# Kernel optimization log

Measured on AMD Instinct MI355X. Metric: run time of the kernel, lower is better.

The kernel has to match this reference:

```python
import jax, jax.numpy as jnp
import numpy as np

N = 4096     # nagents
OBS = 256    # obs_size
HID = 256    # hid_size
G = 64       # gat_hid_size
H1 = 4       # gat_num_heads (so H1*G == HID)
H2 = 1       # gat_num_heads_out
A = 64       # actions
QMAX = 255.0  # 2**quant_bits - 1, quant_min = 0
NEG_SLOPE = 0.2


def _lstm_cell(x, h, c, Wih, Whh, bih, bhh):
    gates = x @ Wih.T + bih + h @ Whh.T + bhh
    i, f, g, o = jnp.split(gates, 4, axis=-1)
    c2 = jax.nn.sigmoid(f) * c + jax.nn.sigmoid(i) * jnp.tanh(g)
    h2 = jax.nn.sigmoid(o) * jnp.tanh(c2)
    return h2, c2


def _gat(x, adj, W, a_i, a_j, b, average, self_loop_type):
    # x: [n, in], adj: [n, n], W: [in, H*g], a_i/a_j: [H, g], b: [H*g] or [g_out]
    n = x.shape[0]
    H, g = a_i.shape
    eye = jnp.eye(n, dtype=adj.dtype)
    if self_loop_type == 1:      # force self-loops
        adj = adj * (1.0 - eye) + eye
    elif self_loop_type == 2:    # remove self-loops
        adj = adj * (1.0 - eye)
    h = (x @ W).reshape(n, H, g)                      # [n, H, g]
    ci = jnp.einsum('nhg,hg->hn', h, a_i)             # [H, n]
    cj = jnp.einsum('nhg,hg->hn', h, a_j)             # [H, n]
    e = jax.nn.leaky_relu(ci[:, :, None] + cj[:, None, :], NEG_SLOPE)  # [H, n, n]
    att = jax.nn.softmax(jnp.where(adj[None] > 0, e, -9e15), axis=-1) * adj[None]
    out = jnp.einsum('hij,jhg->ihg', att, h)          # [n, H, g]
    out = out.mean(axis=1) if average else out.reshape(n, H * g)
    return out + b


def _fake_quant(t, bmask):
    # dynamic-range fake quantization over masked entries (min/max detached)
    big = jnp.asarray(1e30, t.dtype)
    mn = jax.lax.stop_gradient(jnp.min(jnp.where(bmask, t, big)))
    mx = jax.lax.stop_gradient(jnp.max(jnp.where(bmask, t, -big)))
    eq = mn == mx
    mn = jnp.where(eq, mn - 0.01, mn)
    mx = jnp.where(eq, mx + 0.01, mx)
    scale = (mx - mn) / QMAX
    zp = jnp.round(-mn / scale)  # quant_min = 0
    deq = (jnp.clip(jnp.round(t / scale + zp), 0.0, QMAX) - zp) * scale
    return jnp.where(bmask, deq, t)


def _qloss(t, bmask):
    return jnp.sum(jnp.where(bmask, jnp.log2(2.0 * QMAX * jnp.abs(t) + 1.0), 0.0))


def _forward(obs, h0, c0, Wobs, bobs, Wih, Whh, bih, bhh,
             W1, ai1, aj1, b1, W2, ai2, aj2, b2, Wv, bv, Wa, ba):
    n = N
    mask = jnp.ones((n, 1), obs.dtype)        # all agents alive
    enc = obs.reshape(n, -1) @ Wobs + bobs    # obs encoder, squeeze batch=1
    h, c = _lstm_cell(enc, h0, c0, Wih, Whh, bih, bhh)
    comm = h
    bmask = jnp.broadcast_to(mask > 0, comm.shape)
    comm = _fake_quant(comm, bmask)
    loss = _qloss(comm, bmask)
    comm = comm * mask
    adj = jnp.ones((n, n), obs.dtype) * mask * mask.T   # complete graph
    comm = _gat(comm, adj, W1, ai1, aj1, b1, average=False, self_loop_type=1)
    comm = jax.nn.elu(comm)
    bmask2 = jnp.broadcast_to(mask > 0, comm.shape)
    comm = _fake_quant(comm, bmask2)
    loss = loss + _qloss(comm, bmask2)
    comm = _gat(comm, adj, W2, ai2, aj2, b2, average=True, self_loop_type=1)
    comm = comm * mask
    value = jnp.concatenate([h, comm], axis=-1) @ Wv + bv              # [n, 1]
    feat = jnp.concatenate([h.reshape(1, n, -1), comm.reshape(1, n, -1)], axis=-1)
    logp = jax.nn.log_softmax(feat @ Wa + ba, axis=-1)                 # [1, n, A]
    return logp, value, h, c, loss


def setup_inputs() -> dict:
    key = jax.random.key(0)
    ks = jax.random.split(key, 21)
    def rn(k, shape, sc=0.05):
        return jax.random.normal(k, shape, dtype=jnp.float32) * sc
    return {
        'obs': rn(ks[0], (1, N, OBS), 1.0),
        'h0': rn(ks[1], (N, HID), 1.0),
        'c0': rn(ks[2], (N, HID), 1.0),
        'Wobs': rn(ks[3], (OBS, HID)),
        'bobs': rn(ks[4], (HID,)),
        'Wih': rn(ks[5], (4 * HID, HID)),
        'Whh': rn(ks[6], (4 * HID, HID)),
        'bih': rn(ks[7], (4 * HID,)),
        'bhh': rn(ks[8], (4 * HID,)),
        'W1': rn(ks[9], (HID, H1 * G)),
        'ai1': rn(ks[10], (H1, G)),
        'aj1': rn(ks[11], (H1, G)),
        'b1': rn(ks[12], (H1 * G,)),
        'W2': rn(ks[13], (H1 * G, H2 * HID)),
        'ai2': rn(ks[14], (H2, HID)),
        'aj2': rn(ks[15], (H2, HID)),
        'b2': rn(ks[16], (HID,)),
        'Wv': rn(ks[17], (2 * HID, 1)),
        'bv': rn(ks[18], (1,)),
        'Wa': rn(ks[19], (2 * HID, A)),
        'ba': rn(ks[20], (A,)),
    }


def reference(obs, h0, c0, Wobs, bobs, Wih, Whh, bih, bhh,
              W1, ai1, aj1, b1, W2, ai2, aj2, b2, Wv, bv, Wa, ba):
    return _forward(obs, h0, c0, Wobs, bobs, Wih, Whh, bih, bhh,
                    W1, ai1, aj1, b1, W2, ai2, aj2, b2, Wv, bv, Wa, ba)
```

## Files before the change

kernel.cpp:

```cpp
#include <hip/hip_runtime.h>
#include <math.h>

typedef __attribute__((ext_vector_type(8))) short short8;
typedef __attribute__((ext_vector_type(4))) float floatx4;

__device__ __forceinline__ ushort f2b(float f) {
  unsigned u = __float_as_uint(f);
  unsigned r = u + 0x7FFFu + ((u >> 16) & 1u);
  return (ushort)(r >> 16);
}

__global__ __launch_bounds__(256) void prep_kernel(
    const float* __restrict__ obs, ushort* __restrict__ obs_bf,
    const float* __restrict__ h0, ushort* __restrict__ h0_bf,
    const float* __restrict__ Wih, ushort* __restrict__ Wih_bf,
    const float* __restrict__ Whh, ushort* __restrict__ Whh_bf,
    const float* __restrict__ Wobs, ushort* __restrict__ WobsT,
    const float* __restrict__ W1, ushort* __restrict__ W1T,
    const float* __restrict__ W2, ushort* __restrict__ W2T,
    const float* __restrict__ Wa, const float* __restrict__ Wv,
    const float* __restrict__ ba, const float* __restrict__ bv,
    const float* __restrict__ bih, const float* __restrict__ bhh,
    ushort* __restrict__ WaTe, float* __restrict__ bias_ext, float* __restrict__ bias12)
{
  __shared__ float tile[32][33];
  const int bid = blockIdx.x;
  const int tid = threadIdx.x;
  if (bid < 1024) {
    const int q0 = 262144, q1 = 262144, q2 = 65536, q3 = 65536;
    const int tot = q0 + q1 + q2 + q3;
    for (int idx = bid * 256 + tid; idx < tot; idx += 1024 * 256) {
      const float* s; ushort* d; size_t soff, doff; int i = idx;
      if (i < q0) { s = obs; d = obs_bf; soff = doff = (size_t)i * 4; }
      else if ((i -= q0) < q1) { s = h0; d = h0_bf; soff = doff = (size_t)i * 4; }
      else if ((i -= q1) < q2) {
        const int pr = i >> 6, k4 = i & 63;
        const int orow = (pr & 3) * 256 + (pr >> 2);
        s = Wih; d = Wih_bf; soff = (size_t)orow * 256 + k4 * 4; doff = (size_t)pr * 256 + k4 * 4;
      } else {
        i -= q2;
        const int pr = i >> 6, k4 = i & 63;
        const int orow = (pr & 3) * 256 + (pr >> 2);
        s = Whh; d = Whh_bf; soff = (size_t)orow * 256 + k4 * 4; doff = (size_t)pr * 256 + k4 * 4;
      }
      const float4 v = *(const float4*)(s + soff);
      ushort4 o; o.x = f2b(v.x); o.y = f2b(v.y); o.z = f2b(v.z); o.w = f2b(v.w);
      *(ushort4*)(d + doff) = o;
    }
  } else if (bid < 1216) {
    const int t = bid - 1024;
    const int mat = t >> 6, sub = t & 63;
    const float* in = mat == 0 ? Wobs : (mat == 1 ? W1 : W2);
    ushort* outp = mat == 0 ? WobsT : (mat == 1 ? W1T : W2T);
    const int c0 = (sub & 7) * 32, r0 = (sub >> 3) * 32;
    const int tx = tid & 31, ty = tid >> 5;
    #pragma unroll
    for (int p = 0; p < 32; p += 8)
      tile[ty + p][tx] = in[(size_t)(r0 + ty + p) * 256 + c0 + tx];
    __syncthreads();
    #pragma unroll
    for (int p = 0; p < 32; p += 8)
      outp[(size_t)(c0 + ty + p) * 256 + r0 + tx] = f2b(tile[tx][ty + p]);
  } else {
    const int idx = (bid - 1216) * 256 + tid;
    if (idx < 65536) {
      const int n = idx >> 9, k = idx & 511;
      const float v = n < 64 ? Wa[(size_t)k * 64 + n] : (n == 64 ? Wv[k] : 0.0f);
      WaTe[idx] = f2b(v);
    } else if (idx < 65536 + 128) {
      const int n = idx - 65536;
      bias_ext[n] = n < 64 ? ba[n] : (n == 64 ? bv[0] : 0.0f);
    } else if (idx < 65536 + 128 + 1024) {
      const int pc = idx - 65536 - 128;
      const int orow = (pc & 3) * 256 + (pc >> 2);
      bias12[pc] = bih[orow] + bhh[orow];
    }
  }
}

template<int BM, int BN, bool OUT_BF16>
__global__ __launch_bounds__(256) void mfma_gemm(
    const ushort* __restrict__ A1, int lda1,
    const ushort* __restrict__ B1, int ldb1, int K1,
    const ushort* __restrict__ A2, int lda2,
    const ushort* __restrict__ B2, int ldb2, int K2,
    const float* __restrict__ bias,
    void* __restrict__ Cv, int N)
{
  constexpr int LDT = 40;
  __shared__ __align__(16) ushort As[BM * LDT];
  __shared__ __align__(16) ushort Bs[BN * LDT];
  const int tid = threadIdx.x;
  const int wave = tid >> 6, lane = tid & 63;
  const int wr = wave >> 1, wc = wave & 1;
  const int m0 = blockIdx.y * BM, n0 = blockIdx.x * BN;
  constexpr int MI = BM / 32;
  constexpr int NI = BN / 32;
  floatx4 acc[MI][NI] = {};
  const int r = tid >> 2, kq = tid & 3;
  const int lm = lane & 15, lq = lane >> 4;
  const int Ktot = K1 + K2;
  for (int k0 = 0; k0 < Ktot; k0 += 32) {
    const ushort* A; const ushort* B; int lda, ldb, kk;
    if (k0 < K1) { A = A1; B = B1; lda = lda1; ldb = ldb1; kk = k0; }
    else         { A = A2; B = B2; lda = lda2; ldb = ldb2; kk = k0 - K1; }
    #pragma unroll
    for (int p = 0; p < BM / 64; ++p) {
      const int rr = r + p * 64;
      *(float4*)&As[rr * LDT + kq * 8] =
          *(const float4*)&A[(size_t)(m0 + rr) * lda + kk + kq * 8];
    }
    #pragma unroll
    for (int p = 0; p < BN / 64; ++p) {
      const int rr = r + p * 64;
      *(float4*)&Bs[rr * LDT + kq * 8] =
          *(const float4*)&B[(size_t)(n0 + rr) * ldb + kk + kq * 8];
    }
    __syncthreads();
    short8 af[MI], bfr[NI];
    #pragma unroll
    for (int i = 0; i < MI; ++i)
      af[i] = *(const short8*)&As[(wr * (BM / 2) + i * 16 + lm) * LDT + lq * 8];
    #pragma unroll
    for (int j = 0; j < NI; ++j)
      bfr[j] = *(const short8*)&Bs[(wc * (BN / 2) + j * 16 + lm) * LDT + lq * 8];
    #pragma unroll
    for (int i = 0; i < MI; ++i)
      #pragma unroll
      for (int j = 0; j < NI; ++j)
        acc[i][j] = __builtin_amdgcn_mfma_f32_16x16x32_bf16(af[i], bfr[j], acc[i][j], 0, 0, 0);
    __syncthreads();
  }
  #pragma unroll
  for (int i = 0; i < MI; ++i) {
    #pragma unroll
    for (int j = 0; j < NI; ++j) {
      const int col = n0 + wc * (BN / 2) + j * 16 + lm;
      const float badd = bias ? bias[col] : 0.0f;
      #pragma unroll
      for (int t = 0; t < 4; ++t) {
        const int row = m0 + wr * (BM / 2) + i * 16 + lq * 4 + t;
        const float v = acc[i][j][t] + badd;
        if (OUT_BF16) ((ushort*)Cv)[(size_t)row * N + col] = f2b(v);
        else          ((float*)Cv)[(size_t)row * N + col] = v;
      }
    }
  }
}

__global__ __launch_bounds__(256) void gates_lstm_kernel(
    const ushort* __restrict__ enc_bf, const ushort* __restrict__ Wihp,
    const ushort* __restrict__ h0_bf, const ushort* __restrict__ Whhp,
    const float* __restrict__ bias12p, const float* __restrict__ c0,
    float* __restrict__ h_out, float* __restrict__ c_out, ushort* __restrict__ h_bf,
    float* __restrict__ pmn, float* __restrict__ pmx)
{
  constexpr int LDT = 40;
  __shared__ __align__(16) ushort As[128 * LDT];
  __shared__ __align__(16) ushort Bs[128 * LDT];
  __shared__ __align__(16) float gbuf[64][132];
  __shared__ float smn[4], smx[4];
  const int tid = threadIdx.x;
  const int wave = tid >> 6, lane = tid & 63;
  const int wr = wave >> 1, wc = wave & 1;
  const int m0 = blockIdx.y * 128, n0 = blockIdx.x * 128;
  floatx4 acc[4][4] = {};
  const int r = tid >> 2, kq = tid & 3;
  const int lm = lane & 15, lq = lane >> 4;
  for (int k0 = 0; k0 < 512; k0 += 32) {
    const ushort* A; const ushort* B; int kk;
    if (k0 < 256) { A = enc_bf; B = Wihp; kk = k0; }
    else          { A = h0_bf;  B = Whhp; kk = k0 - 256; }
    #pragma unroll
    for (int p = 0; p < 2; ++p) {
      const int rr = r + p * 64;
      *(float4*)&As[rr * LDT + kq * 8] =
          *(const float4*)&A[(size_t)(m0 + rr) * 256 + kk + kq * 8];
      *(float4*)&Bs[rr * LDT + kq * 8] =
          *(const float4*)&B[(size_t)(n0 + rr) * 256 + kk + kq * 8];
    }
    __syncthreads();
    short8 af[4], bfr[4];
    #pragma unroll
    for (int i = 0; i < 4; ++i)
      af[i] = *(const short8*)&As[(wr * 64 + i * 16 + lm) * LDT + lq * 8];
    #pragma unroll
    for (int j = 0; j < 4; ++j)
      bfr[j] = *(const short8*)&Bs[(wc * 64 + j * 16 + lm) * LDT + lq * 8];
    #pragma unroll
    for (int i = 0; i < 4; ++i)
      #pragma unroll
      for (int j = 0; j < 4; ++j)
        acc[i][j] = __builtin_amdgcn_mfma_f32_16x16x32_bf16(af[i], bfr[j], acc[i][j], 0, 0, 0);
    __syncthreads();
  }
  float mnl = 3.0e38f, mxl = -3.0e38f;
  const int rr = tid >> 2;
  const int dd0 = (tid & 3) * 8;
  #pragma unroll
  for (int half = 0; half < 2; ++half) {
    if (wr == half) {
      #pragma unroll
      for (int i = 0; i < 4; ++i)
        #pragma unroll
        for (int j = 0; j < 4; ++j) {
          const int col = wc * 64 + j * 16 + lm;
          const float badd = bias12p[n0 + col];
          #pragma unroll
          for (int t = 0; t < 4; ++t)
            gbuf[i * 16 + lq * 4 + t][col] = acc[i][j][t] + badd;
        }
    }
    __syncthreads();
    const int ig = m0 + half * 64 + rr;
    #pragma unroll
    for (int eh = 0; eh < 2; ++eh) {
      const int ddb = dd0 + eh * 4;
      const size_t off = (size_t)ig * 256 + (n0 >> 2) + ddb;
      const float4 c4 = *(const float4*)&c0[off];
      float4 hv, cv; ushort4 hb;
      #pragma unroll
      for (int q = 0; q < 4; ++q) {
        const float4 g4 = *(const float4*)&gbuf[rr][(ddb + q) * 4];
        const float cc = ((const float*)&c4)[q];
        const float si = 1.0f / (1.0f + expf(-g4.x));
        const float sf = 1.0f / (1.0f + expf(-g4.y));
        const float so = 1.0f / (1.0f + expf(-g4.w));
        const float c2 = sf * cc + si * tanhf(g4.z);
        const float h2 = so * tanhf(c2);
        ((float*)&hv)[q] = h2; ((float*)&cv)[q] = c2; ((ushort*)&hb)[q] = f2b(h2);
        mnl = fminf(mnl, h2); mxl = fmaxf(mxl, h2);
      }
      *(float4*)&h_out[off] = hv;
      *(float4*)&c_out[off] = cv;
      *(ushort4*)&h_bf[off] = hb;
    }
    __syncthreads();
  }
  #pragma unroll
  for (int o = 32; o > 0; o >>= 1) {
    mnl = fminf(mnl, __shfl_xor(mnl, o));
    mxl = fmaxf(mxl, __shfl_xor(mxl, o));
  }
  if (lane == 0) { smn[wave] = mnl; smx[wave] = mxl; }
  __syncthreads();
  if (tid == 0) {
    const int bid = blockIdx.y * 8 + blockIdx.x;
    pmn[bid] = fminf(fminf(smn[0], smn[1]), fminf(smn[2], smn[3]));
    pmx[bid] = fmaxf(fmaxf(smx[0], smx[1]), fmaxf(smx[2], smx[3]));
  }
}

// ... 33 lines not shown
      d1 = (qq - zp) * scale; lsum += log2f(510.0f * fabsf(d1) + 1.0f); }
    { float qq = fminf(fmaxf(rintf(t.z / scale + zp), 0.0f), 255.0f);
      d2 = (qq - zp) * scale; lsum += log2f(510.0f * fabsf(d2) + 1.0f); }
    { float qq = fminf(fmaxf(rintf(t.w / scale + zp), 0.0f), 255.0f);
      d3 = (qq - zp) * scale; lsum += log2f(510.0f * fabsf(d3) + 1.0f); }
    ushort4 o; o.x = f2b(d0); o.y = f2b(d1); o.z = f2b(d2); o.w = f2b(d3);
    *(ushort4*)(q + (size_t)idx * 4) = o;
  }
  #pragma unroll
  for (int o = 32; o > 0; o >>= 1) lsum += __shfl_xor(lsum, o);
  if ((threadIdx.x & 63) == 0) sl[threadIdx.x >> 6] = lsum;
  __syncthreads();
  if (threadIdx.x == 0) part[blockIdx.x] = sl[0] + sl[1] + sl[2] + sl[3];
}

__global__ __launch_bounds__(256) void cicj1_kernel(
    const float* __restrict__ h1, const float* __restrict__ ai, const float* __restrict__ aj,
    float* __restrict__ ci, float* __restrict__ cj)
{
  const int w = threadIdx.x >> 6, lane = threadIdx.x & 63;
  const int i = blockIdx.x * 4 + w;
  #pragma unroll
  for (int hd = 0; hd < 4; ++hd) {
    const float v = h1[(size_t)i * 256 + hd * 64 + lane];
    float pi = v * ai[hd * 64 + lane];
    float pj = v * aj[hd * 64 + lane];
    #pragma unroll
    for (int o = 32; o > 0; o >>= 1) { pi += __shfl_xor(pi, o); pj += __shfl_xor(pj, o); }
    if (lane == 0) { ci[hd * 4096 + i] = pi; cj[hd * 4096 + i] = pj; }
  }
}

__global__ __launch_bounds__(256) void cicj2_kernel(
    const float* __restrict__ h2, const float* __restrict__ ai, const float* __restrict__ aj,
    float* __restrict__ ci, float* __restrict__ cj)
{
  const int w = threadIdx.x >> 6, lane = threadIdx.x & 63;
  const int i = blockIdx.x * 4 + w;
  float pi = 0.f, pj = 0.f;
  #pragma unroll
  for (int r = 0; r < 4; ++r) {
    const float v = h2[(size_t)i * 256 + r * 64 + lane];
    pi += v * ai[r * 64 + lane];
    pj += v * aj[r * 64 + lane];
  }
  #pragma unroll
  for (int o = 32; o > 0; o >>= 1) { pi += __shfl_xor(pi, o); pj += __shfl_xor(pj, o); }
  if (lane == 0) { ci[i] = pi; cj[i] = pj; }
}

__global__ __launch_bounds__(1024) void rank_sort_kernel(
    const float* __restrict__ c, float* __restrict__ sc, int* __restrict__ pm)
{
  __shared__ unsigned long long lk[4096];
  __shared__ int scnt[16][64];
  const int head = blockIdx.x >> 6;
  const int seg = blockIdx.x & 63;
  const float* ch = c + head * 4096;
  for (int idx = threadIdx.x; idx < 4096; idx += 1024) {
    unsigned u = __float_as_uint(ch[idx]);
    u = (u & 0x80000000u) ? ~u : (u | 0x80000000u);
    lk[idx] = ((unsigned long long)u << 12) | (unsigned)idx;
  }
  __syncthreads();
  const int jl = threadIdx.x & 63;
  const int kg = threadIdx.x >> 6;
  const unsigned long long my = lk[seg * 64 + jl];
  int cnt = 0;
  const int k0 = kg * 256;
  #pragma unroll 8
  for (int k = k0; k < k0 + 256; ++k)
    cnt += lk[k] < my ? 1 : 0;
  scnt[kg][jl] = cnt;
  __syncthreads();
  if (threadIdx.x < 64) {
    int rank = 0;
    #pragma unroll
    for (int g = 0; g < 16; ++g) rank += scnt[g][threadIdx.x];
    const unsigned long long kk = lk[seg * 64 + threadIdx.x];
    unsigned u = (unsigned)(kk >> 12);
    const float v = __uint_as_float((u & 0x80000000u) ? (u & 0x7fffffffu) : ~u);
    sc[head * 4096 + rank] = v;
    pm[head * 4096 + rank] = (int)(kk & 0xFFFu);
  }
}

__global__ __launch_bounds__(128) void local_scan1(
    const float* __restrict__ h1, const float* __restrict__ sc, const int* __restrict__ pm,
    float* __restrict__ PUl, float* __restrict__ PVl,
    float* __restrict__ dUl, float* __restrict__ dVl,
    float* __restrict__ cku, float* __restrict__ ckv,
    float* __restrict__ ckus, float* __restrict__ ckvs)
{
  const int head = blockIdx.x >> 6;
  const int chunk = blockIdx.x & 63;
  const int wave = threadIdx.x >> 6;
  const int lane = threadIdx.x & 63;
  const float cmax = sc[head * 4096 + 4095];
// ... 153 lines not shown
    const float us = ckus[lane];
    float iv = vs, iu = us;
    #pragma unroll
    for (int o = 1; o < 64; o <<= 1) {
      const float tv = __shfl_up(iv, o), tu = __shfl_up(iu, o);
      if (lane >= o) { iv += tv; iu += tu; }
    }
    prefVs[lane] = iv - vs;
    const float totU = __shfl(iu, 63);
    sufUs[lane] = totU - iu + us;
    if (lane == 63) { prefVs[64] = iv; sufUs[64] = 0.f; }
  }
}

__global__ __launch_bounds__(256) void combine1_kernel(
    const float* __restrict__ ci, const float* __restrict__ sc,
    const float* __restrict__ sufU, const float* __restrict__ prefV,
    const float* __restrict__ sufUs, const float* __restrict__ prefVs,
    const float* __restrict__ PUl, const float* __restrict__ PVl,
    const float* __restrict__ dUl, const float* __restrict__ dVl,
    const float* __restrict__ b1, float* __restrict__ out,
    float* __restrict__ pmn, float* __restrict__ pmx)
{
  const int i = blockIdx.x;
  const int head = threadIdx.x >> 6;
  const int lane = threadIdx.x & 63;
  const float* sch = sc + head * 4096;
  const float civ = ci[head * 4096 + i];
  const float cmax = sch[4095];
  const float sarg = civ + cmax;
  const float m = sarg > 0.f ? sarg : 0.2f * sarg;
  const float Af = expf(sarg - m);
  const float Bf = expf(0.2f * sarg - m);
  const float t = -civ;
  int lo = 0, hi = 4096;
  while (lo < hi) {
    const int mid = (lo + hi) >> 1;
    if (sch[mid] > t) hi = mid; else lo = mid + 1;
  }
  const int s = lo;
  float accP, accN, dP, dN;
  if (s == 4096) {
    accP = 0.f; dP = 0.f;
    accN = prefV[(head * 65 + 64) * 64 + lane];
    dN = prefVs[head * 65 + 64];
  } else {
    const int cs = s >> 6;
    accP = sufU[(head * 65 + cs + 1) * 64 + lane] + PUl[(size_t)(head * 4096 + s) * 64 + lane];
    accN = prefV[(head * 65 + cs) * 64 + lane] + PVl[(size_t)(head * 4096 + s) * 64 + lane];
    dP = sufUs[head * 65 + cs + 1] + dUl[head * 4096 + s];
    dN = prefVs[head * 65 + cs] + dVl[head * 4096 + s];
  }
  const float num = Af * accP + Bf * accN;
// ... 5 lines not shown
  #pragma unroll
  for (int of = 32; of > 0; of >>= 1) {
    mn = fminf(mn, __shfl_xor(mn, of));
    mx = fmaxf(mx, __shfl_xor(mx, of));
  }
  __shared__ float smn[4], smx[4];
  if (lane == 0) { smn[head] = mn; smx[head] = mx; }
  __syncthreads();
  if (threadIdx.x == 0) {
    pmn[i] = fminf(fminf(smn[0], smn[1]), fminf(smn[2], smn[3]));
    pmx[i] = fmaxf(fmaxf(smx[0], smx[1]), fmaxf(smx[2], smx[3]));
  }
}

__global__ __launch_bounds__(256) void combine2_kernel(
    const float* __restrict__ ci, const float* __restrict__ sc,
    const float* __restrict__ sufU, const float* __restrict__ prefV,
    const float* __restrict__ sufUs, const float* __restrict__ prefVs,
    const float* __restrict__ PUl, const float* __restrict__ PVl,
    const float* __restrict__ dUl, const float* __restrict__ dVl,
    const float* __restrict__ b2, ushort* __restrict__ outb)
{
  const int i = blockIdx.x;
  const int col = threadIdx.x;
  const float civ = ci[i];
  const float cmax = sc[4095];
  const float sarg = civ + cmax;
  const float m = sarg > 0.f ? sarg : 0.2f * sarg;
  const float Af = expf(sarg - m);
  const float Bf = expf(0.2f * sarg - m);
  const float t = -civ;
  int lo = 0, hi = 4096;
  while (lo < hi) {
    const int mid = (lo + hi) >> 1;
    if (sc[mid] > t) hi = mid; else lo = mid + 1;
  }
  const int s = lo;
  float accP, accN, dP, dN;
  if (s == 4096) {
    accP = 0.f; dP = 0.f;
    accN = prefV[64 * 256 + col];
    dN = prefVs[64];
  } else {
    const int cs = s >> 6;
    accP = sufU[(cs + 1) * 256 + col] + PUl[(size_t)s * 256 + col];
    accN = prefV[cs * 256 + col] + PVl[(size_t)s * 256 + col];
    dP = sufUs[cs + 1] + dUl[s];
    dN = prefVs[cs] + dVl[s];
  }
  const float num = Af * accP + Bf * accN;
// ... 107 lines not shown

  float* out       = (float*)d_out;
  float* out_logp  = out;
  float* out_value = out + 262144;
  float* out_h     = out + 266240;
  float* out_c     = out + 1314816;
  float* out_loss  = out + 2363392;

  char* ws = (char*)d_ws;
  float* part1  = (float*)(ws + 256);
  float* part2  = (float*)(ws + 1280);
  float* pmn    = (float*)(ws + 2304);
  float* pmx    = (float*)(ws + 18688);
  const size_t MB = 1048576;
  const size_t base = 35072;
  ushort* obs_bf  = (ushort*)(ws + base);
  ushort* h0_bf   = (ushort*)(ws + base + 2 * MB);
  ushort* Wih_bf  = (ushort*)(ws + base + 4 * MB);
  ushort* Whh_bf  = (ushort*)(ws + base + 4 * MB + 524288);
  ushort* WobsT   = (ushort*)(ws + base + 5 * MB);
  ushort* W1T     = (ushort*)(ws + base + 5 * MB + 131072);
  ushort* W2T     = (ushort*)(ws + base + 5 * MB + 262144);
  ushort* WaTe    = (ushort*)(ws + base + 5 * MB + 393216);
  float*  bias_ext= (float*) (ws + base + 5 * MB + 524288);
  float*  bias12  = (float*) (ws + base + 5 * MB + 525312);
  ushort* enc_bf  = (ushort*)(ws + base + 6 * MB);
  ushort* h_bf    = (ushort*)(ws + base + 8 * MB);
  ushort* comm_q1 = (ushort*)(ws + base + 10 * MB);
  ushort* comm_q2 = (ushort*)(ws + base + 12 * MB);
  ushort* comm2_bf= (ushort*)(ws + base + 14 * MB);
  float*  scratch = (float*) (ws + base + 16 * MB);
  float*  h1      = scratch;
  float*  comm1e  = (float*)((char*)scratch + 4 * MB);
  float*  h2b     = (float*)((char*)scratch + 8 * MB);
  size_t so = base + 32 * MB;
  auto alloc = [&](size_t bytes) { size_t r = so; so += (bytes + 255) & ~255ull; return (char*)ws + r; };
  float* ci1    = (float*)alloc(4 * 4096 * 4);
  float* cj1    = (float*)alloc(4 * 4096 * 4);
  float* sc1    = (float*)alloc(4 * 4096 * 4);
  int*   pm1    = (int*)  alloc(4 * 4096 * 4);
  float* cku1   = (float*)alloc(4 * 64 * 64 * 4);
  float* ckv1   = (float*)alloc(4 * 64 * 64 * 4);
  float* ckus1  = (float*)alloc(4 * 64 * 4);
  float* ckvs1  = (float*)alloc(4 * 64 * 4);
  float* sufU1  = (float*)alloc(4 * 65 * 64 * 4);
  float* prefV1 = (float*)alloc(4 * 65 * 64 * 4);
  float* sufUs1 = (float*)alloc(4 * 65 * 4);
  float* prefVs1= (float*)alloc(4 * 65 * 4);
  float* ci2    = (float*)alloc(4096 * 4);
  float* cj2    = (float*)alloc(4096 * 4);
  float* sc2    = (float*)alloc(4096 * 4);
  int*   pm2    = (int*)  alloc(4096 * 4);
  float* cku2   = (float*)alloc(64 * 256 * 4);
  float* ckv2   = (float*)alloc(64 * 256 * 4);
  float* ckus2  = (float*)alloc(64 * 4);
  float* ckvs2  = (float*)alloc(64 * 4);
  float* sufU2  = (float*)alloc(65 * 256 * 4);
  float* prefV2 = (float*)alloc(65 * 256 * 4);
  float* sufUs2 = (float*)alloc(65 * 4);
  float* prefVs2= (float*)alloc(65 * 4);
  float* PUl    = (float*)alloc(4 * 4096 * 64 * 4);
  float* PVl    = (float*)alloc(4 * 4096 * 64 * 4);
  float* dUl    = (float*)alloc(4 * 4096 * 4);
  float* dVl    = (float*)alloc(4 * 4096 * 4);

  const dim3 b256(256);
  const int N4 = 262144;

  prep_kernel<<<dim3(1477), b256, 0, stream>>>(
      obs, obs_bf, h0, h0_bf, Wih, Wih_bf, Whh, Whh_bf,
      Wobs, WobsT, W1, W1T, W2, W2T,
      Wa, Wv, ba, bv, bih, bhh, WaTe, bias_ext, bias12);
  mfma_gemm<64, 64, true><<<dim3(4, 64), b256, 0, stream>>>(
      obs_bf, 256, WobsT, 256, 256, nullptr, 0, nullptr, 0, 0, bobs, enc_bf, 256);
  gates_lstm_kernel<<<dim3(8, 32), b256, 0, stream>>>(
      enc_bf, Wih_bf, h0_bf, Whh_bf, bias12, c0, out_h, out_c, h_bf, pmn, pmx);
  quant_kernel<<<dim3(256), b256, 0, stream>>>(
      (const float4*)out_h, comm_q1, N4, pmn, pmx, 256, part1);
  mfma_gemm<64, 64, false><<<dim3(4, 64), b256, 0, stream>>>(
      comm_q1, 256, W1T, 256, 256, nullptr, 0, nullptr, 0, 0, nullptr, h1, 256);
  cicj1_kernel<<<dim3(1024), b256, 0, stream>>>(h1, ai1, aj1, ci1, cj1);
  rank_sort_kernel<<<dim3(256), dim3(1024), 0, stream>>>(cj1, sc1, pm1);
  local_scan1<<<dim3(256), dim3(128), 0, stream>>>(h1, sc1, pm1,
      PUl, PVl, dUl, dVl, cku1, ckv1, ckus1, ckvs1);
  prefix1_kernel<<<dim3(4), dim3(64), 0, stream>>>(cku1, ckv1, ckus1, ckvs1,
                                                   sufU1, prefV1, sufUs1, prefVs1);
  combine1_kernel<<<dim3(4096), b256, 0, stream>>>(ci1, sc1,
      sufU1, prefV1, sufUs1, prefVs1, PUl, PVl, dUl, dVl, b1, comm1e, pmn, pmx);
  quant_kernel<<<dim3(256), b256, 0, stream>>>(
      (const float4*)comm1e, comm_q2, N4, pmn, pmx, 4096, part2);
  mfma_gemm<64, 64, false><<<dim3(4, 64), b256, 0, stream>>>(
      comm_q2, 256, W2T, 256, 256, nullptr, 0, nullptr, 0, 0, nullptr, h2b, 256);
  cicj2_kernel<<<dim3(1024), b256, 0, stream>>>(h2b, ai2, aj2, ci2, cj2);
  rank_sort_kernel<<<dim3(64), dim3(1024), 0, stream>>>(cj2, sc2, pm2);
  local_scan2<<<dim3(2, 64), b256, 0, stream>>>(h2b, sc2, pm2,
      PUl, PVl, dUl, dVl, cku2, ckv2, ckus2, ckvs2);
  prefix2_kernel<<<dim3(1), b256, 0, stream>>>(cku2, ckv2, ckus2, ckvs2,
                                               sufU2, prefV2, sufUs2, prefVs2);
  combine2_kernel<<<dim3(4096), b256, 0, stream>>>(ci2, sc2,
      sufU2, prefV2, sufUs2, prefVs2, PUl, PVl, dUl, dVl, b2, comm2_bf);
  heads_kernel<<<dim3(64), b256, 0, stream>>>(
      h_bf, comm2_bf, WaTe, bias_ext, out_logp, out_value, part1, part2, out_loss);
}
```

Before: 245.6 us.

## Fuse bf16 casts into GEMMs, fold attention vectors into weights, register LSTM epilogue

The obs and h0 bf16 conversions now happen inside the encoder and gates GEMM tile loads, so the standalone conversion passes and their buffers go away. The attention projection vectors are folded into the GAT weights (W·a) during prep. A new gat_feat kernel then computes the features and the ci/cj coefficients together, which removes the separate cicj kernels. The gate weight permutation is changed so each lane holds all four gates in registers, dropping the shared-memory gbuf epilogue. The sort now emits integer keys so the combine binary search compares unsigned keys. This risks small numeric differences, because ci/cj now come from bf16-folded weights instead of the fp32 features.

```diff
diff --git a/kernel.cpp b/kernel.cpp
--- a/kernel.cpp
+++ b/kernel.cpp
@@ -9,46 +9,44 @@
   unsigned r = u + 0x7FFFu + ((u >> 16) & 1u);
   return (ushort)(r >> 16);
 }
+__device__ __forceinline__ unsigned encf(float f) {
+  unsigned u = __float_as_uint(f);
+  return (u & 0x80000000u) ? ~u : (u | 0x80000000u);
+}
+__device__ __forceinline__ float b2f(ushort b) {
+  return __uint_as_float(((unsigned)b) << 16);
+}
 
 __global__ __launch_bounds__(256) void prep_kernel(
-    const float* __restrict__ obs, ushort* __restrict__ obs_bf,
-    const float* __restrict__ h0, ushort* __restrict__ h0_bf,
-    const float* __restrict__ Wih, ushort* __restrict__ Wih_bf,
-    const float* __restrict__ Whh, ushort* __restrict__ Whh_bf,
+    const float* __restrict__ Wih, ushort* __restrict__ Wihp,
+    const float* __restrict__ Whh, ushort* __restrict__ Whhp,
     const float* __restrict__ Wobs, ushort* __restrict__ WobsT,
     const float* __restrict__ W1, ushort* __restrict__ W1T,
     const float* __restrict__ W2, ushort* __restrict__ W2T,
     const float* __restrict__ Wa, const float* __restrict__ Wv,
     const float* __restrict__ ba, const float* __restrict__ bv,
     const float* __restrict__ bih, const float* __restrict__ bhh,
-    ushort* __restrict__ WaTe, float* __restrict__ bias_ext, float* __restrict__ bias12)
+    ushort* __restrict__ WaTe, float* __restrict__ bias_ext, float* __restrict__ bias12,
+    const float* __restrict__ ai1, const float* __restrict__ aj1,
+    const float* __restrict__ ai2, const float* __restrict__ aj2,
+    ushort* __restrict__ wab1, ushort* __restrict__ wab2)
 {
   __shared__ float tile[32][33];
   const int bid = blockIdx.x;
   const int tid = threadIdx.x;
-  if (bid < 1024) {
-    const int q0 = 262144, q1 = 262144, q2 = 65536, q3 = 65536;
-    const int tot = q0 + q1 + q2 + q3;
-    for (int idx = bid * 256 + tid; idx < tot; idx += 1024 * 256) {
-      const float* s; ushort* d; size_t soff, doff; int i = idx;
-      if (i < q0) { s = obs; d = obs_bf; soff = doff = (size_t)i * 4; }
-      else if ((i -= q0) < q1) { s = h0; d = h0_bf; soff = doff = (size_t)i * 4; }
-      else if ((i -= q1) < q2) {
-        const int pr = i >> 6, k4 = i & 63;
-        const int orow = (pr & 3) * 256 + (pr >> 2);
-        s = Wih; d = Wih_bf; soff = (size_t)orow * 256 + k4 * 4; doff = (size_t)pr * 256 + k4 * 4;
-      } else {
-        i -= q2;
-        const int pr = i >> 6, k4 = i & 63;
-        const int orow = (pr & 3) * 256 + (pr >> 2);
-        s = Whh; d = Whh_bf; soff = (size_t)orow * 256 + k4 * 4; doff = (size_t)pr * 256 + k4 * 4;
-      }
-      const float4 v = *(const float4*)(s + soff);
-      ushort4 o; o.x = f2b(v.x); o.y = f2b(v.y); o.z = f2b(v.z); o.w = f2b(v.w);
-      *(ushort4*)(d + doff) = o;
-    }
-  } else if (bid < 1216) {
-    const int t = bid - 1024;
+  if (bid < 512) {
+    const int i = bid * 256 + tid;
+    const int half = i >> 16;
+    const int ii = i & 65535;
+    const int pr = ii >> 6, k4 = ii & 63;
+    const int orow = ((pr >> 4) & 3) * 256 + (pr >> 6) * 16 + (pr & 15);
+    const float* s = half ? Whh : Wih;
+    ushort* d = half ? Whhp : Wihp;
+    const float4 v = *(const float4*)(s + (size_t)orow * 256 + k4 * 4);
+    ushort4 o; o.x = f2b(v.x); o.y = f2b(v.y); o.z = f2b(v.z); o.w = f2b(v.w);
+    *(ushort4*)(d + (size_t)pr * 256 + k4 * 4) = o;
+  } else if (bid < 704) {
+    const int t = bid - 512;
     const int mat = t >> 6, sub = t & 63;
     const float* in = mat == 0 ? Wobs : (mat == 1 ? W1 : W2);
     ushort* outp = mat == 0 ? WobsT : (mat == 1 ? W1T : W2T);
@@ -61,8 +59,8 @@
     #pragma unroll
     for (int p = 0; p < 32; p += 8)
       outp[(size_t)(c0 + ty + p) * 256 + r0 + tx] = f2b(tile[tx][ty + p]);
-  } else {
-    const int idx = (bid - 1216) * 256 + tid;
+  } else if (bid < 965) {
+    const int idx = (bid - 704) * 256 + tid;
     if (idx < 65536) {
       const int n = idx >> 9, k = idx & 511;
       const float v = n < 64 ? Wa[(size_t)k * 64 + n] : (n == 64 ? Wv[k] : 0.0f);
@@ -72,85 +70,92 @@
       bias_ext[n] = n < 64 ? ba[n] : (n == 64 ? bv[0] : 0.0f);
     } else if (idx < 65536 + 128 + 1024) {
       const int pc = idx - 65536 - 128;
-      const int orow = (pc & 3) * 256 + (pc >> 2);
+      const int orow = ((pc >> 4) & 3) * 256 + (pc >> 6) * 16 + (pc & 15);
       bias12[pc] = bih[orow] + bhh[orow];
     }
-  }
-}
-
-template<int BM, int BN, bool OUT_BF16>
-__global__ __launch_bounds__(256) void mfma_gemm(
-    const ushort* __restrict__ A1, int lda1,
-    const ushort* __restrict__ B1, int ldb1, int K1,
-    const ushort* __restrict__ A2, int lda2,
-    const ushort* __restrict__ B2, int ldb2, int K2,
-    const float* __restrict__ bias,
-    void* __restrict__ Cv, int N)
+  } else if (bid < 981) {
+    const int c = bid - 965;
+    const int k = tid;
+    float val = 0.0f;
+    if (c < 8) {
+      const int h = c & 3;
+      const float* av = (c < 4) ? ai1 : aj1;
+      for (int g = 0; g < 64; ++g)
+        val += W1[(size_t)k * 256 + h * 64 + g] * av[h * 64 + g];
+    }
+    wab1[c * 256 + k] = f2b(val);
+  } else {
+    const int c = bid - 981;
+    const int k = tid;
+    float val = 0.0f;
+    if (c < 2) {
+      const float* av = (c == 0) ? ai2 : aj2;
+      for (int g = 0; g < 256; ++g)
+        val += W2[(size_t)k * 256 + g] * av[g];
+    }
+    wab2[c * 256 + k] = f2b(val);
+  }
+}
+
+__global__ __launch_bounds__(256) void enc_gemm(
+    const float* __restrict__ obs, const ushort* __restrict__ WobsT,
+    const float* __restrict__ bobs, ushort* __restrict__ enc_bf)
 {
   constexpr int LDT = 40;
-  __shared__ __align__(16) ushort As[BM * LDT];
-  __shared__ __align__(16) ushort Bs[BN * LDT];
+  __shared__ __align__(16) ushort As[64 * LDT];
+  __shared__ __align__(16) ushort Bs[64 * LDT];
   const int tid = threadIdx.x;
   const int wave = tid >> 6, lane = tid & 63;
   const int wr = wave >> 1, wc = wave & 1;
-  const int m0 = blockIdx.y * BM, n0 = blockIdx.x * BN;
-  constexpr int MI = BM / 32;
-  constexpr int NI = BN / 32;
-  floatx4 acc[MI][NI] = {};
+  const int m0 = blockIdx.y * 64, n0 = blockIdx.x * 64;
+  floatx4 acc[2][2] = {};
   const int r = tid >> 2, kq = tid & 3;
   const int lm = lane & 15, lq = lane >> 4;
-  const int Ktot = K1 + K2;
-  for (int k0 = 0; k0 < Ktot; k0 += 32) {
-    const ushort* A; const ushort* B; int lda, ldb, kk;
-    if (k0 < K1) { A = A1; B = B1; lda = lda1; ldb = ldb1; kk = k0; }
-    else         { A = A2; B = B2; lda = lda2; ldb = ldb2; kk = k0 - K1; }
-    #pragma unroll
-    for (int p = 0; p < BM / 64; ++p) {
-      const int rr = r + p * 64;
-      *(float4*)&As[rr * LDT + kq * 8] =
-          *(const float4*)&A[(size_t)(m0 + rr) * lda + kk + kq * 8];
-    }
-    #pragma unroll
-    for (int p = 0; p < BN / 64; ++p) {
-      const int rr = r + p * 64;
-      *(float4*)&Bs[rr * LDT + kq * 8] =
-          *(const float4*)&B[(size_t)(n0 + rr) * ldb + kk + kq * 8];
+  for (int k0 = 0; k0 < 256; k0 += 32) {
+    {
+      const float* s = &obs[(size_t)(m0 + r) * 256 + k0 + kq * 8];
+      const float4 a = *(const float4*)s;
+      const float4 b = *(const float4*)(s + 4);
+      ushort4 o1, o2;
+      o1.x = f2b(a.x); o1.y = f2b(a.y); o1.z = f2b(a.z); o1.w = f2b(a.w);
+      o2.x = f2b(b.x); o2.y = f2b(b.y); o2.z = f2b(b.z); o2.w = f2b(b.w);
+      *(ushort4*)&As[r * LDT + kq * 8] = o1;
+      *(ushort4*)&As[r * LDT + kq * 8 + 4] = o2;
+      *(float4*)&Bs[r * LDT + kq * 8] =
+          *(const float4*)&WobsT[(size_t)(n0 + r) * 256 + k0 + kq * 8];
     }
     __syncthreads();
-    short8 af[MI], bfr[NI];
-    #pragma unroll
-    for (int i = 0; i < MI; ++i)
-      af[i] = *(const short8*)&As[(wr * (BM / 2) + i * 16 + lm) * LDT + lq * 8];
-    #pragma unroll
-    for (int j = 0; j < NI; ++j)
-      bfr[j] = *(const short8*)&Bs[(wc * (BN / 2) + j * 16 + lm) * LDT + lq * 8];
-    #pragma unroll
-    for (int i = 0; i < MI; ++i)
-      #pragma unroll
-      for (int j = 0; j < NI; ++j)
+    short8 af[2], bfr[2];
+    #pragma unroll
+    for (int i = 0; i < 2; ++i)
+      af[i] = *(const short8*)&As[(wr * 32 + i * 16 + lm) * LDT + lq * 8];
+    #pragma unroll
+    for (int j = 0; j < 2; ++j)
+      bfr[j] = *(const short8*)&Bs[(wc * 32 + j * 16 + lm) * LDT + lq * 8];
+    #pragma unroll
+    for (int i = 0; i < 2; ++i)
+      #pragma unroll
+      for (int j = 0; j < 2; ++j)
         acc[i][j] = __builtin_amdgcn_mfma_f32_16x16x32_bf16(af[i], bfr[j], acc[i][j], 0, 0, 0);
     __syncthreads();
   }
   #pragma unroll
-  for (int i = 0; i < MI; ++i) {
-    #pragma unroll
-    for (int j = 0; j < NI; ++j) {
-      const int col = n0 + wc * (BN / 2) + j * 16 + lm;
-      const float badd = bias ? bias[col] : 0.0f;
+  for (int i = 0; i < 2; ++i)
+    #pragma unroll
+    for (int j = 0; j < 2; ++j) {
+      const int col = n0 + wc * 32 + j * 16 + lm;
+      const float badd = bobs[col];
       #pragma unroll
       for (int t = 0; t < 4; ++t) {
-        const int row = m0 + wr * (BM / 2) + i * 16 + lq * 4 + t;
-        const float v = acc[i][j][t] + badd;
-        if (OUT_BF16) ((ushort*)Cv)[(size_t)row * N + col] = f2b(v);
-        else          ((float*)Cv)[(size_t)row * N + col] = v;
+        const int row = m0 + wr * 32 + i * 16 + lq * 4 + t;
+        enc_bf[(size_t)row * 256 + col] = f2b(acc[i][j][t] + badd);
       }
     }
-  }
 }
 
 __global__ __launch_bounds__(256) void gates_lstm_kernel(
     const ushort* __restrict__ enc_bf, const ushort* __restrict__ Wihp,
-    const ushort* __restrict__ h0_bf, const ushort* __restrict__ Whhp,
+    const float* __restrict__ h0, const ushort* __restrict__ Whhp,
     const float* __restrict__ bias12p, const float* __restrict__ c0,
     float* __restrict__ h_out, float* __restrict__ c_out, ushort* __restrict__ h_bf,
     float* __restrict__ pmn, float* __restrict__ pmx)
@@ -158,7 +163,6 @@
   constexpr int LDT = 40;
   __shared__ __align__(16) ushort As[128 * LDT];
   __shared__ __align__(16) ushort Bs[128 * LDT];
-  __shared__ __align__(16) float gbuf[64][132];
   __shared__ float smn[4], smx[4];
   const int tid = threadIdx.x;
   const int wave = tid >> 6, lane = tid & 63;
@@ -168,14 +172,32 @@
   const int r = tid >> 2, kq = tid & 3;
   const int lm = lane & 15, lq = lane >> 4;
   for (int k0 = 0; k0 < 512; k0 += 32) {
-    const ushort* A; const ushort* B; int kk;
-    if (k0 < 256) { A = enc_bf; B = Wihp; kk = k0; }
-    else          { A = h0_bf;  B = Whhp; kk = k0 - 256; }
+    const ushort* B = (k0 < 256) ? Wihp : Whhp;
+    const int kk = (k0 < 256) ? k0 : k0 - 256;
+    if (k0 < 256) {
+      #pragma unroll
+      for (int p = 0; p < 2; ++p) {
+        const int rr = r + p * 64;
+        *(float4*)&As[rr * LDT + kq * 8] =
+            *(const float4*)&enc_bf[(size_t)(m0 + rr) * 256 + kk + kq * 8];
+      }
+    } else {
+      #pragma unroll
+      for (int p = 0; p < 2; ++p) {
+        const int rr = r + p * 64;
+        const float* s = &h0[(size_t)(m0 + rr) * 256 + kk + kq * 8];
+        const float4 a = *(const float4*)s;
+        const float4 b = *(const float4*)(s + 4);
+        ushort4 o1, o2;
+        o1.x = f2b(a.x); o1.y = f2b(a.y); o1.z = f2b(a.z); o1.w = f2b(a.w);
+        o2.x = f2b(b.x); o2.y = f2b(b.y); o2.z = f2b(b.z); o2.w = f2b(b.w);
+        *(ushort4*)&As[rr * LDT + kq * 8] = o1;
+        *(ushort4*)&As[rr * LDT + kq * 8 + 4] = o2;
+      }
+    }
     #pragma unroll
     for (int p = 0; p < 2; ++p) {
       const int rr = r + p * 64;
-      *(float4*)&As[rr * LDT + kq * 8] =
-          *(const float4*)&A[(size_t)(m0 + rr) * 256 + kk + kq * 8];
       *(float4*)&Bs[rr * LDT + kq * 8] =
           *(const float4*)&B[(size_t)(n0 + rr) * 256 + kk + kq * 8];
     }
@@ -194,48 +216,32 @@
         acc[i][j] = __builtin_amdgcn_mfma_f32_16x16x32_bf16(af[i], bfr[j], acc[i][j], 0, 0, 0);
     __syncthreads();
   }
+  const int d = (blockIdx.x * 2 + wc) * 16 + lm;
+  float b4[4];
+  #pragma unroll
+  for (int j = 0; j < 4; ++j) b4[j] = bias12p[n0 + wc * 64 + j * 16 + lm];
   float mnl = 3.0e38f, mxl = -3.0e38f;
-  const int rr = tid >> 2;
-  const int dd0 = (tid & 3) * 8;
   #pragma unroll
-  for (int half = 0; half < 2; ++half) {
-    if (wr == half) {
-      #pragma unroll
-      for (int i = 0; i < 4; ++i)
-        #pragma unroll
-        for (int j = 0; j < 4; ++j) {
-          const int col = wc * 64 + j * 16 + lm;
-          const float badd = bias12p[n0 + col];
-          #pragma unroll
-          for (int t = 0; t < 4; ++t)
-            gbuf[i * 16 + lq * 4 + t][col] = acc[i][j][t] + badd;
-        }
-    }
-    __syncthreads();
-    const int ig = m0 + half * 64 + rr;
-    #pragma unroll
-    for (int eh = 0; eh < 2; ++eh) {
-      const int ddb = dd0 + eh * 4;
-      const size_t off = (size_t)ig * 256 + (n0 >> 2) + ddb;
-      const float4 c4 = *(const float4*)&c0[off];
-      float4 hv, cv; ushort4 hb;
-      #pragma unroll
-      for (int q = 0; q < 4; ++q) {
-        const float4 g4 = *(const float4*)&gbuf[rr][(ddb + q) * 4];
-        const float cc = ((const float*)&c4)[q];
-        const float si = 1.0f / (1.0f + expf(-g4.x));
-        const float sf = 1.0f / (1.0f + expf(-g4.y));
-        const float so = 1.0f / (1.0f + expf(-g4.w));
-        const float c2 = sf * cc + si * tanhf(g4.z);
-        const float h2 = so * tanhf(c2);
-        ((float*)&hv)[q] = h2; ((float*)&cv)[q] = c2; ((ushort*)&hb)[q] = f2b(h2);
-        mnl = fminf(mnl, h2); mxl = fmaxf(mxl, h2);
-      }
-      *(float4*)&h_out[off] = hv;
-      *(float4*)&c_out[off] = cv;
-      *(ushort4*)&h_bf[off] = hb;
-    }
-    __syncthreads();
+  for (int i = 0; i < 4; ++i) {
+    #pragma unroll
+    for (int t = 0; t < 4; ++t) {
+      const int row = m0 + wr * 64 + i * 16 + lq * 4 + t;
+      const size_t off = (size_t)row * 256 + d;
+      const float gi = acc[i][0][t] + b4[0];
+      const float gf = acc[i][1][t] + b4[1];
+      const float gg = acc[i][2][t] + b4[2];
+      const float go = acc[i][3][t] + b4[3];
+      const float cc = c0[off];
+      const float si = 1.0f / (1.0f + expf(-gi));
+      const float sf = 1.0f / (1.0f + expf(-gf));
+      const float so = 1.0f / (1.0f + expf(-go));
+      const float c2 = sf * cc + si * tanhf(gg);
+      const float h2 = so * tanhf(c2);
+      h_out[off] = h2;
+      c_out[off] = c2;
+      h_bf[off] = f2b(h2);
+      mnl = fminf(mnl, h2); mxl = fmaxf(mxl, h2);
+    }
   }
   #pragma unroll
   for (int o = 32; o > 0; o >>= 1) {
@@ -299,58 +305,95 @@
   if (threadIdx.x == 0) part[blockIdx.x] = sl[0] + sl[1] + sl[2] + sl[3];
 }
 
-__global__ __launch_bounds__(256) void cicj1_kernel(
-    const float* __restrict__ h1, const float* __restrict__ ai, const float* __restrict__ aj,
-    float* __restrict__ ci, float* __restrict__ cj)
-{
-  const int w = threadIdx.x >> 6, lane = threadIdx.x & 63;
-  const int i = blockIdx.x * 4 + w;
-  #pragma unroll
-  for (int hd = 0; hd < 4; ++hd) {
-    const float v = h1[(size_t)i * 256 + hd * 64 + lane];
-    float pi = v * ai[hd * 64 + lane];
-    float pj = v * aj[hd * 64 + lane];
-    #pragma unroll
-    for (int o = 32; o > 0; o >>= 1) { pi += __shfl_xor(pi, o); pj += __shfl_xor(pj, o); }
-    if (lane == 0) { ci[hd * 4096 + i] = pi; cj[hd * 4096 + i] = pj; }
-  }
-}
-
-__global__ __launch_bounds__(256) void cicj2_kernel(
-    const float* __restrict__ h2, const float* __restrict__ ai, const float* __restrict__ aj,
-    float* __restrict__ ci, float* __restrict__ cj)
-{
-  const int w = threadIdx.x >> 6, lane = threadIdx.x & 63;
-  const int i = blockIdx.x * 4 + w;
-  float pi = 0.f, pj = 0.f;
-  #pragma unroll
-  for (int r = 0; r < 4; ++r) {
-    const float v = h2[(size_t)i * 256 + r * 64 + lane];
-    pi += v * ai[r * 64 + lane];
-    pj += v * aj[r * 64 + lane];
-  }
-  #pragma unroll
-  for (int o = 32; o > 0; o >>= 1) { pi += __shfl_xor(pi, o); pj += __shfl_xor(pj, o); }
-  if (lane == 0) { ci[i] = pi; cj[i] = pj; }
+template<int HN>
+__global__ __launch_bounds__(256) void gat_feat_kernel(
+    const ushort* __restrict__ Aq, const ushort* __restrict__ WT,
+    const ushort* __restrict__ wab,
+    float* __restrict__ hout, float* __restrict__ ci, float* __restrict__ cj)
+{
+  constexpr int LDT = 40;
+  __shared__ __align__(16) ushort As[64 * LDT];
+  __shared__ __align__(16) ushort Bs[64 * LDT];
+  const int bid = blockIdx.x;
+  const int tid = threadIdx.x;
+  const int wave = tid >> 6, lane = tid & 63;
+  const int lm = lane & 15, lq = lane >> 4;
+  const int r = tid >> 2, kq = tid & 3;
+  if (bid < 256) {
+    const int bx = bid & 3, by = bid >> 2;
+    const int m0 = by * 64, n0 = bx * 64;
+    const int wr = wave >> 1, wc = wave & 1;
+    floatx4 acc[2][2] = {};
+    for (int k0 = 0; k0 < 256; k0 += 32) {
+      *(float4*)&As[r * LDT + kq * 8] =
+          *(const float4*)&Aq[(size_t)(m0 + r) * 256 + k0 + kq * 8];
+      *(float4*)&Bs[r * LDT + kq * 8] =
+          *(const float4*)&WT[(size_t)(n0 + r) * 256 + k0 + kq * 8];
+      __syncthreads();
+      short8 af[2], bfr[2];
+      #pragma unroll
+      for (int i = 0; i < 2; ++i)
+        af[i] = *(const short8*)&As[(wr * 32 + i * 16 + lm) * LDT + lq * 8];
+      #pragma unroll
+      for (int j = 0; j < 2; ++j)
+        bfr[j] = *(const short8*)&Bs[(wc * 32 + j * 16 + lm) * LDT + lq * 8];
+      #pragma unroll
+      for (int i = 0; i < 2; ++i)
+        #pragma unroll
+        for (int j = 0; j < 2; ++j)
+          acc[i][j] = __builtin_amdgcn_mfma_f32_16x16x32_bf16(af[i], bfr[j], acc[i][j], 0, 0, 0);
+      __syncthreads();
+    }
+    #pragma unroll
+    for (int i = 0; i < 2; ++i)
+      #pragma unroll
+      for (int j = 0; j < 2; ++j) {
+        const int col = n0 + wc * 32 + j * 16 + lm;
+        #pragma unroll
+        for (int t = 0; t < 4; ++t) {
+          const int row = m0 + wr * 32 + i * 16 + lq * 4 + t;
+          hout[(size_t)row * 256 + col] = acc[i][j][t];
+        }
+      }
+  } else {
+    const int m0 = (bid - 256) * 64;
+    floatx4 acc = {0.f, 0.f, 0.f, 0.f};
+    for (int k0 = 0; k0 < 256; k0 += 32) {
+      *(float4*)&As[r * LDT + kq * 8] =
+          *(const float4*)&Aq[(size_t)(m0 + r) * 256 + k0 + kq * 8];
+      if (r < 16)
+        *(float4*)&Bs[r * LDT + kq * 8] =
+            *(const float4*)&wab[(size_t)r * 256 + k0 + kq * 8];
+      __syncthreads();
+      const short8 af = *(const short8*)&As[(wave * 16 + lm) * LDT + lq * 8];
+      const short8 bf = *(const short8*)&Bs[lm * LDT + lq * 8];
+      acc = __builtin_amdgcn_mfma_f32_16x16x32_bf16(af, bf, acc, 0, 0, 0);
+      __syncthreads();
+    }
+    #pragma unroll
+    for (int t = 0; t < 4; ++t) {
+      const int row = m0 + wave * 16 + lq * 4 + t;
+      if (lm < HN) ci[lm * 4096 + row] = acc[t];
+      else if (lm < 2 * HN) cj[(lm - HN) * 4096 + row] = acc[t];
+    }
+  }
 }
 
 __global__ __launch_bounds__(1024) void rank_sort_kernel(
-    const float* __restrict__ c, float* __restrict__ sc, int* __restrict__ pm)
-{
-  __shared__ unsigned long long lk[4096];
+    const float* __restrict__ c, unsigned* __restrict__ skey,
+    float* __restrict__ sc, int* __restrict__ pm)
+{
+  __shared__ unsigned lk[4096];
   __shared__ int scnt[16][64];
   const int head = blockIdx.x >> 6;
   const int seg = blockIdx.x & 63;
   const float* ch = c + head * 4096;
-  for (int idx = threadIdx.x; idx < 4096; idx += 1024) {
-    unsigned u = __float_as_uint(ch[idx]);
-    u = (u & 0x80000000u) ? ~u : (u | 0x80000000u);
-    lk[idx] = ((unsigned long long)u << 12) | (unsigned)idx;
-  }
+  for (int idx = threadIdx.x; idx < 4096; idx += 1024)
+    lk[idx] = (encf(ch[idx]) & 0xFFFFF000u) | (unsigned)idx;
   __syncthreads();
   const int jl = threadIdx.x & 63;
   const int kg = threadIdx.x >> 6;
-  const unsigned long long my = lk[seg * 64 + jl];
+  const unsigned my = lk[seg * 64 + jl];
   int cnt = 0;
   const int k0 = kg * 256;
   #pragma unroll 8
@@ -362,11 +405,11 @@
     int rank = 0;
     #pragma unroll
     for (int g = 0; g < 16; ++g) rank += scnt[g][threadIdx.x];
-    const unsigned long long kk = lk[seg * 64 + threadIdx.x];
-    unsigned u = (unsigned)(kk >> 12);
-    const float v = __uint_as_float((u & 0x80000000u) ? (u & 0x7fffffffu) : ~u);
-    sc[head * 4096 + rank] = v;
-    pm[head * 4096 + rank] = (int)(kk & 0xFFFu);
+    const unsigned kk = lk[seg * 64 + threadIdx.x];
+    const int jj = (int)(kk & 0xFFFu);
+    skey[head * 4096 + rank] = kk;
+    sc[head * 4096 + rank] = ch[jj];
+    pm[head * 4096 + rank] = jj;
   }
 }
 
@@ -550,7 +593,8 @@
 }
 
 __global__ __launch_bounds__(256) void combine1_kernel(
-    const float* __restrict__ ci, const float* __restrict__ sc,
+    const float* __restrict__ ci, const unsigned* __restrict__ skey,
+    const float* __restrict__ sc,
     const float* __restrict__ sufU, const float* __restrict__ prefV,
     const float* __restrict__ sufUs, const float* __restrict__ prefVs,
     const float* __restrict__ PUl, const float* __restrict__ PVl,
@@ -561,18 +605,18 @@
   const int i = blockIdx.x;
   const int head = threadIdx.x >> 6;
   const int lane = threadIdx.x & 63;
-  const float* sch = sc + head * 4096;
+  const unsigned* skh = skey + head * 4096;
   const float civ = ci[head * 4096 + i];
-  const float cmax = sch[4095];
+  const float cmax = sc[head * 4096 + 4095];
   const float sarg = civ + cmax;
   const float m = sarg > 0.f ? sarg : 0.2f * sarg;
   const float Af = expf(sarg - m);
   const float Bf = expf(0.2f * sarg - m);
-  const float t = -civ;
+  const unsigned tkey = (encf(-civ) & 0xFFFFF000u) | 0xFFFu;
   int lo = 0, hi = 4096;
   while (lo < hi) {
     const int mid = (lo + hi) >> 1;
-    if (sch[mid] > t) hi = mid; else lo = mid + 1;
+    if (skh[mid] > tkey) hi = mid; else lo = mid + 1;
   }
   const int s = lo;
   float accP, accN, dP, dN;
@@ -608,7 +652,8 @@
 }
 
 __global__ __launch_bounds__(256) void combine2_kernel(
-    const float* __restrict__ ci, const float* __restrict__ sc,
+    const float* __restrict__ ci, const unsigned* __restrict__ skey,
+    const float* __restrict__ sc,
     const float* __restrict__ sufU, const float* __restrict__ prefV,
     const float* __restrict__ sufUs, const float* __restrict__ prefVs,
     const float* __restrict__ PUl, const float* __restrict__ PVl,
@@ -623,11 +668,11 @@
   const float m = sarg > 0.f ? sarg : 0.2f * sarg;
   const float Af = expf(sarg - m);
   const float Bf = expf(0.2f * sarg - m);
-  const float t = -civ;
+  const unsigned tkey = (encf(-civ) & 0xFFFFF000u) | 0xFFFu;
   int lo = 0, hi = 4096;
   while (lo < hi) {
     const int mid = (lo + hi) >> 1;
-    if (sc[mid] > t) hi = mid; else lo = mid + 1;
+    if (skey[mid] > tkey) hi = mid; else lo = mid + 1;
   }
   const int s = lo;
   float accP, accN, dP, dN;
@@ -765,29 +810,29 @@
   float* pmx    = (float*)(ws + 18688);
   const size_t MB = 1048576;
   const size_t base = 35072;
-  ushort* obs_bf  = (ushort*)(ws + base);
-  ushort* h0_bf   = (ushort*)(ws + base + 2 * MB);
-  ushort* Wih_bf  = (ushort*)(ws + base + 4 * MB);
-  ushort* Whh_bf  = (ushort*)(ws + base + 4 * MB + 524288);
-  ushort* WobsT   = (ushort*)(ws + base + 5 * MB);
-  ushort* W1T     = (ushort*)(ws + base + 5 * MB + 131072);
-  ushort* W2T     = (ushort*)(ws + base + 5 * MB + 262144);
-  ushort* WaTe    = (ushort*)(ws + base + 5 * MB + 393216);
-  float*  bias_ext= (float*) (ws + base + 5 * MB + 524288);
-  float*  bias12  = (float*) (ws + base + 5 * MB + 525312);
-  ushort* enc_bf  = (ushort*)(ws + base + 6 * MB);
-  ushort* h_bf    = (ushort*)(ws + base + 8 * MB);
-  ushort* comm_q1 = (ushort*)(ws + base + 10 * MB);
-  ushort* comm_q2 = (ushort*)(ws + base + 12 * MB);
-  ushort* comm2_bf= (ushort*)(ws + base + 14 * MB);
-  float*  scratch = (float*) (ws + base + 16 * MB);
-  float*  h1      = scratch;
-  float*  comm1e  = (float*)((char*)scratch + 4 * MB);
-  float*  h2b     = (float*)((char*)scratch + 8 * MB);
-  size_t so = base + 32 * MB;
+  ushort* Wihp    = (ushort*)(ws + base);
+  ushort* Whhp    = (ushort*)(ws + base + 524288);
+  ushort* WobsT   = (ushort*)(ws + base + 1 * MB);
+  ushort* W1T     = (ushort*)(ws + base + 1 * MB + 131072);
+  ushort* W2T     = (ushort*)(ws + base + 1 * MB + 262144);
+  ushort* WaTe    = (ushort*)(ws + base + 1 * MB + 393216);
+  float*  bias_ext= (float*) (ws + base + 1 * MB + 524288);
+  float*  bias12  = (float*) (ws + base + 1 * MB + 525312);
+  ushort* wab1    = (ushort*)(ws + base + 1 * MB + 532480);
+  ushort* wab2    = (ushort*)(ws + base + 1 * MB + 540672);
+  ushort* enc_bf  = (ushort*)(ws + base + 2 * MB);
+  ushort* h_bf    = (ushort*)(ws + base + 4 * MB);
+  ushort* comm_q1 = (ushort*)(ws + base + 6 * MB);
+  ushort* comm_q2 = (ushort*)(ws + base + 8 * MB);
+  ushort* comm2_bf= (ushort*)(ws + base + 10 * MB);
+  float*  h1      = (float*) (ws + base + 12 * MB);
+  float*  comm1e  = (float*) (ws + base + 16 * MB);
+  float*  h2b     = (float*) (ws + base + 20 * MB);
+  size_t so = base + 24 * MB;
   auto alloc = [&](size_t bytes) { size_t r = so; so += (bytes + 255) & ~255ull; return (char*)ws + r; };
   float* ci1    = (float*)alloc(4 * 4096 * 4);
   float* cj1    = (float*)alloc(4 * 4096 * 4);
+  unsigned* skey1 = (unsigned*)alloc(4 * 4096 * 4);
   float* sc1    = (float*)alloc(4 * 4096 * 4);
   int*   pm1    = (int*)  alloc(4 * 4096 * 4);
   float* cku1   = (float*)alloc(4 * 64 * 64 * 4);
@@ -800,6 +845,7 @@
   float* prefVs1= (float*)alloc(4 * 65 * 4);
   float* ci2    = (float*)alloc(4096 * 4);
   float* cj2    = (float*)alloc(4096 * 4);
+  unsigned* skey2 = (unsigned*)alloc(4096 * 4);
   float* sc2    = (float*)alloc(4096 * 4);
   int*   pm2    = (int*)  alloc(4096 * 4);
   float* cku2   = (float*)alloc(64 * 256 * 4);
@@ -818,37 +864,34 @@
   const dim3 b256(256);
   const int N4 = 262144;
 
-  prep_kernel<<<dim3(1477), b256, 0, stream>>>(
-      obs, obs_bf, h0, h0_bf, Wih, Wih_bf, Whh, Whh_bf,
-      Wobs, WobsT, W1, W1T, W2, W2T,
-      Wa, Wv, ba, bv, bih, bhh, WaTe, bias_ext, bias12);
-  mfma_gemm<64, 64, true><<<dim3(4, 64), b256, 0, stream>>>(
-      obs_bf, 256, WobsT, 256, 256, nullptr, 0, nullptr, 0, 0, bobs, enc_bf, 256);
+  prep_kernel<<<dim3(997), b256, 0, stream>>>(
+      Wih, Wihp, Whh, Whhp, Wobs, WobsT, W1, W1T, W2, W2T,
+      Wa, Wv, ba, bv, bih, bhh, WaTe, bias_ext, bias12,
+      ai1, aj1, ai2, aj2, wab1, wab2);
+  enc_gemm<<<dim3(4, 64), b256, 0, stream>>>(obs, WobsT, bobs, enc_bf);
   gates_lstm_kernel<<<dim3(8, 32), b256, 0, stream>>>(
-      enc_bf, Wih_bf, h0_bf, Whh_bf, bias12, c0, out_h, out_c, h_bf, pmn, pmx);
+      enc_bf, Wihp, h0, Whhp, bias12, c0, out_h, out_c, h_bf, pmn, pmx);
   quant_kernel<<<dim3(256), b256, 0, stream>>>(
       (const float4*)out_h, comm_q1, N4, pmn, pmx, 256, part1);
-  mfma_gemm<64, 64, false><<<dim3(4, 64), b256, 0, stream>>>(
-      comm_q1, 256, W1T, 256, 256, nullptr, 0, nullptr, 0, 0, nullptr, h1, 256);
-  cicj1_kernel<<<dim3(1024), b256, 0, stream>>>(h1, ai1, aj1, ci1, cj1);
-  rank_sort_kernel<<<dim3(256), dim3(1024), 0, stream>>>(cj1, sc1, pm1);
+  gat_feat_kernel<4><<<dim3(320), b256, 0, stream>>>(
+      comm_q1, W1T, wab1, h1, ci1, cj1);
+  rank_sort_kernel<<<dim3(256), dim3(1024), 0, stream>>>(cj1, skey1, sc1, pm1);
   local_scan1<<<dim3(256), dim3(128), 0, stream>>>(h1, sc1, pm1,
       PUl, PVl, dUl, dVl, cku1, ckv1, ckus1, ckvs1);
   prefix1_kernel<<<dim3(4), dim3(64), 0, stream>>>(cku1, ckv1, ckus1, ckvs1,
                                                    sufU1, prefV1, sufUs1, prefVs1);
-  combine1_kernel<<<dim3(4096), b256, 0, stream>>>(ci1, sc1,
+  combine1_kernel<<<dim3(4096), b256, 0, stream>>>(ci1, skey1, sc1,
       sufU1, prefV1, sufUs1, prefVs1, PUl, PVl, dUl, dVl, b1, comm1e, pmn, pmx);
   quant_kernel<<<dim3(256), b256, 0, stream>>>(
       (const float4*)comm1e, comm_q2, N4, pmn, pmx, 4096, part2);
-  mfma_gemm<64, 64, false><<<dim3(4, 64), b256, 0, stream>>>(
-      comm_q2, 256, W2T, 256, 256, nullptr, 0, nullptr, 0, 0, nullptr, h2b, 256);
-  cicj2_kernel<<<dim3(1024), b256, 0, stream>>>(h2b, ai2, aj2, ci2, cj2);
-  rank_sort_kernel<<<dim3(64), dim3(1024), 0, stream>>>(cj2, sc2, pm2);
+  gat_feat_kernel<1><<<dim3(320), b256, 0, stream>>>(
+      comm_q2, W2T, wab2, h2b, ci2, cj2);
+  rank_sort_kernel<<<dim3(64), dim3(1024), 0, stream>>>(cj2, skey2, sc2, pm2);
   local_scan2<<<dim3(2, 64), b256, 0, stream>>>(h2b, sc2, pm2,
       PUl, PVl, dUl, dVl, cku2, ckv2, ckus2, ckvs2);
   prefix2_kernel<<<dim3(1), b256, 0, stream>>>(cku2, ckv2, ckus2, ckvs2,
                                                sufU2, prefV2, sufUs2, prefVs2);
-  combine2_kernel<<<dim3(4096), b256, 0, stream>>>(ci2, sc2,
+  combine2_kernel<<<dim3(4096), b256, 0, stream>>>(ci2, skey2, sc2,
       sufU2, prefV2, sufUs2, prefVs2, PUl, PVl, dUl, dVl, b2, comm2_bf);
   heads_kernel<<<dim3(64), b256, 0, stream>>>(
       h_bf, comm2_bf, WaTe, bias_ext, out_logp, out_value, part1, part2, out_loss);
```

New measurement: 248.0 us. Within noise of the previous version (+1.0%).
